# Kernel optimization log

Hardware: AMD Instinct MI355X
Metric: run time of the kernel (lower is better)

The kernel has to match this reference:

```python
import jax, jax.numpy as jnp
import numpy as np

B, R, N, D_IN, D_OUT = 8, 8, 1024, 256, 256


def setup_inputs() -> dict:
    key = jax.random.key(0)
    k1, k2, k3, k4 = jax.random.split(key, 4)
    x = jax.random.normal(k1, (B, N, D_IN), dtype=jnp.float32)
    adj_stack = jax.random.uniform(k2, (B, R, N, N), dtype=jnp.float32)
    # per-relation Linear params, stacked: W[r] maps D_IN -> D_OUT
    bound = 1.0 / np.sqrt(D_IN)
    W = jax.random.uniform(k3, (R, D_IN, D_OUT), minval=-bound, maxval=bound, dtype=jnp.float32)
    b = jax.random.uniform(k4, (R, D_OUT), minval=-bound, maxval=bound, dtype=jnp.float32)
    return {"x": x, "adj_stack": adj_stack, "W": W, "b": b}


def reference(x, adj_stack, W, b):
    # support[b,r,n,e] = x[b,n,:] @ W[r] + b[r]
    support = jnp.einsum('bnd,rde->brne', x, W) + b[None, :, None, :]
    # out[b,m,e] = sum_r adj[b,r,m,:] @ support[b,r,:,e]
    out = jnp.einsum('brmn,brne->bme', adj_stack, support)
    return jax.nn.relu(out)
```

## Files before the change

kernel.cpp:

```cpp
#include <hip/hip_runtime.h>
#include <hip/hip_bf16.h>


#define Bb 8
#define Rr 8
#define Nn 1024
#define Dd 256

typedef __attribute__((ext_vector_type(8))) short short8;
typedef __attribute__((ext_vector_type(4))) short short4v;
typedef __attribute__((ext_vector_type(4))) float f32x4;

__device__ __forceinline__ short f2bf(float f) {
    unsigned u = __builtin_bit_cast(unsigned, f);
    u += 0x7fffu + ((u >> 16) & 1u);
    return (short)(u >> 16);
}

__global__ void prep_w_kernel(const float* __restrict__ W, short* __restrict__ Wt) {
    __shared__ short T[64][72];
    const int tid = threadIdx.x;
    const int et = blockIdx.x, dt = blockIdx.y, r = blockIdx.z;
    const float* Wr = W + ((size_t)r * Dd + dt * 64) * Dd + et * 64;
    #pragma unroll
    for (int i = 0; i < 4; ++i) {
        int idx = tid + i * 256;
        int d_l = idx >> 4;
        int e4  = (idx & 15) * 4;
        f32x4 v = *(const f32x4*)(Wr + d_l * Dd + e4);
        T[e4 + 0][d_l] = f2bf(v[0]);
        T[e4 + 1][d_l] = f2bf(v[1]);
        T[e4 + 2][d_l] = f2bf(v[2]);
        T[e4 + 3][d_l] = f2bf(v[3]);
    }
    __syncthreads();
    short* o = Wt + ((size_t)r * Dd + et * 64) * Dd + dt * 64;
    #pragma unroll
    for (int i = 0; i < 2; ++i) {
        int idx = tid + i * 256;
        int e_l = idx >> 3;
        int d8  = (idx & 7) * 8;
        *(short8*)(o + e_l * Dd + d8) = *(const short8*)&T[e_l][d8];
    }
}

__global__ __launch_bounds__(256) void support_kernel(
        const float* __restrict__ x, const short* __restrict__ Wt,
        const float* __restrict__ bias, short* __restrict__ sup) {
    __shared__ short As[128][40];
    __shared__ short Bs[128][40];

    const int tid = threadIdx.x;
    const int e_t = blockIdx.x, n_t = blockIdx.y, br = blockIdx.z;
    const int b = br >> 3, r = br & 7;
    const int wave = tid >> 6, lane = tid & 63;
    const int quad = lane >> 4, l16 = lane & 15;
    const int we = wave & 1, wn = wave >> 1;

    const short* wp = Wt + ((size_t)r * Dd + e_t * 128) * Dd;
    const float* xb = x + ((size_t)b * Nn + n_t * 128) * Dd;

    short8 aw[2];
    f32x4 xv[4];
    auto load = [&](int d0) {
        #pragma unroll
        for (int i = 0; i < 2; ++i) {
            int idx = tid + i * 256;
            aw[i] = *(const short8*)(wp + (idx >> 2) * Dd + d0 + (idx & 3) * 8);
        }
        #pragma unroll
        for (int i = 0; i < 4; ++i) {
            int idx = tid + i * 256;
            xv[i] = *(const f32x4*)(xb + (idx >> 3) * Dd + d0 + (idx & 7) * 4);
        }
    };

    f32x4 acc[4][4] = {};
    load(0);
    for (int it = 0; it < 8; ++it) {
        #pragma unroll
        for (int i = 0; i < 2; ++i) {
            int idx = tid + i * 256;
            *(short8*)&As[idx >> 2][(idx & 3) * 8] = aw[i];
        }
        #pragma unroll
        for (int i = 0; i < 4; ++i) {
            int idx = tid + i * 256;
            short4v s;
            s[0] = f2bf(xv[i][0]); s[1] = f2bf(xv[i][1]);
            s[2] = f2bf(xv[i][2]); s[3] = f2bf(xv[i][3]);
            *(short4v*)&Bs[idx >> 3][(idx & 7) * 4] = s;
        }
        if (it < 7) load((it + 1) * 32);
        __syncthreads();
        short8 a[4], bfr[4];
        #pragma unroll
        for (int i = 0; i < 4; ++i)
            a[i] = *(const short8*)&As[we * 64 + i * 16 + l16][quad * 8];
        #pragma unroll
        for (int j = 0; j < 4; ++j)
            bfr[j] = *(const short8*)&Bs[wn * 64 + j * 16 + l16][quad * 8];
        #pragma unroll
        for (int i = 0; i < 4; ++i)
            #pragma unroll
            for (int j = 0; j < 4; ++j)
                acc[i][j] = __builtin_amdgcn_mfma_f32_16x16x32_bf16(a[i], bfr[j], acc[i][j], 0, 0, 0);
        __syncthreads();
    }

    #pragma unroll
    for (int i = 0; i < 4; ++i)
        #pragma unroll
        for (int reg = 0; reg < 4; ++reg) {
            int e = e_t * 128 + we * 64 + i * 16 + quad * 4 + reg;
            float bv = bias[r * Dd + e];
            #pragma unroll
            for (int j = 0; j < 4; ++j) {
                int n = n_t * 128 + wn * 64 + j * 16 + l16;
                sup[(((b * Rr + r) * Dd + e) << 10) + n] = f2bf(acc[i][j][reg] + bv);
            }
        }
}

__global__ __launch_bounds__(256) void gcn_gemm_kernel(
        const float* __restrict__ adj, const short* __restrict__ sup,
        float* __restrict__ out) {
    __shared__ short Aa[128][40];
    __shared__ short Bs[128][40];

    const int tid = threadIdx.x;
    const int e2  = blockIdx.x & 1;
    const int r   = blockIdx.x >> 1;
    const int m_t = blockIdx.y, b = blockIdx.z;
    const int wave = tid >> 6, lane = tid & 63;
    const int quad = lane >> 4, l16 = lane & 15;
    const int wm = wave >> 1, we = wave & 1;

    const float* ap = adj + ((size_t)((b * Rr + r) * Nn + m_t * 128)) * Nn;
    const short* bp = sup + (((size_t)((b * Rr + r) * Dd + e2 * 128)) << 10);

    f32x4 av[4];
    short8 bv[2];
    auto load = [&](int n0) {
        #pragma unroll
        for (int i = 0; i < 4; ++i) {
            int idx = tid + i * 256;
            av[i] = *(const f32x4*)(ap + (size_t)(idx >> 3) * Nn + n0 + (idx & 7) * 4);
        }
        #pragma unroll
        for (int i = 0; i < 2; ++i) {
            int idx = tid + i * 256;
            bv[i] = *(const short8*)(bp + ((size_t)(idx >> 2) << 10) + n0 + (idx & 3) * 8);
        }
    };

    f32x4 acc[4][4] = {};
    load(0);
    for (int it = 0; it < 32; ++it) {
        #pragma unroll
        for (int i = 0; i < 4; ++i) {
            int idx = tid + i * 256;
            short4v s;
            s[0] = f2bf(av[i][0]); s[1] = f2bf(av[i][1]);
            s[2] = f2bf(av[i][2]); s[3] = f2bf(av[i][3]);
            *(short4v*)&Aa[idx >> 3][(idx & 7) * 4] = s;
        }
        #pragma unroll
        for (int i = 0; i < 2; ++i) {
            int idx = tid + i * 256;
            *(short8*)&Bs[idx >> 2][(idx & 3) * 8] = bv[i];
        }
        if (it < 31) load((it + 1) * 32);
        __syncthreads();
        short8 a[4], bfr[4];
        #pragma unroll
        for (int i = 0; i < 4; ++i)
            a[i] = *(const short8*)&Aa[wm * 64 + i * 16 + l16][quad * 8];
        #pragma unroll
        for (int j = 0; j < 4; ++j)
            bfr[j] = *(const short8*)&Bs[we * 64 + j * 16 + l16][quad * 8];
        #pragma unroll
        for (int i = 0; i < 4; ++i)
            #pragma unroll
            for (int j = 0; j < 4; ++j)
                acc[i][j] = __builtin_amdgcn_mfma_f32_16x16x32_bf16(a[i], bfr[j], acc[i][j], 0, 0, 0);
        __syncthreads();
    }

    float* ob = out + ((size_t)b * Nn + m_t * 128) * Dd + e2 * 128;
    #pragma unroll
    for (int i = 0; i < 4; ++i)
        #pragma unroll
        for (int reg = 0; reg < 4; ++reg) {
            int m_l = wm * 64 + i * 16 + quad * 4 + reg;
            #pragma unroll
            for (int j = 0; j < 4; ++j) {
                int e_l = we * 64 + j * 16 + l16;
                atomicAdd(ob + (size_t)m_l * Dd + e_l, acc[i][j][reg]);
            }
        }
}

__global__ void relu_kernel(float* __restrict__ out, int n4) {
    int i = blockIdx.x * blockDim.x + threadIdx.x;
    if (i < n4) {
        f32x4* p = (f32x4*)out;
        f32x4 v = p[i];
        v[0] = fmaxf(v[0], 0.f); v[1] = fmaxf(v[1], 0.f);
        v[2] = fmaxf(v[2], 0.f); v[3] = fmaxf(v[3], 0.f);
        p[i] = v;
    }
}

extern "C" void kernel_launch(void* const* d_in, const int* in_sizes, int n_in,
                              void* d_out, int out_size, void* d_ws, size_t ws_size,
                              hipStream_t stream) {
    const float* x    = (const float*)d_in[0];
    const float* adj  = (const float*)d_in[1];
    const float* W    = (const float*)d_in[2];
    const float* bias = (const float*)d_in[3];
    float* out = (float*)d_out;
    short* sup = (short*)d_ws;
    short* Wt  = (short*)d_out;

    prep_w_kernel<<<dim3(4, 4, 8), 256, 0, stream>>>(W, Wt);
    support_kernel<<<dim3(2, 8, 64), 256, 0, stream>>>(x, Wt, bias, sup);
    hipMemsetAsync(d_out, 0, (size_t)out_size * sizeof(float), stream);
    gcn_gemm_kernel<<<dim3(16, 8, 8), 256, 0, stream>>>(adj, sup, out);
    relu_kernel<<<(out_size / 4 + 255) / 256, 256, 0, stream>>>(out, out_size / 4);
}
```

Before: 464.7 us.

## Load MFMA fragments directly from global memory and drop LDS staging

Both GEMM kernels stop staging tiles through shared memory and drop the block barriers. Each wave now loads its A and B fragments from global memory straight into MFMA register layout, converting fp32 to bf16 in registers. Tiles are reshaped so each wave owns a 64-column slice of the output features. In the adjacency GEMM this means all four waves of a block load and convert the same 64x32 adjacency tile, so global/L1 traffic and conversion work are duplicated in exchange for removing LDS writes, LDS reads and barriers.

```diff
diff --git a/kernel.cpp b/kernel.cpp
--- a/kernel.cpp
+++ b/kernel.cpp
@@ -2,13 +2,11 @@
 #include <hip/hip_bf16.h>
 
 
-#define Bb 8
 #define Rr 8
 #define Nn 1024
 #define Dd 256
 
 typedef __attribute__((ext_vector_type(8))) short short8;
-typedef __attribute__((ext_vector_type(4))) short short4v;
 typedef __attribute__((ext_vector_type(4))) float f32x4;
 
 __device__ __forceinline__ short f2bf(float f) {
@@ -38,86 +36,70 @@
     #pragma unroll
     for (int i = 0; i < 2; ++i) {
         int idx = tid + i * 256;
-        int e_l = idx >> 3;
-        int d8  = (idx & 7) * 8;
-        *(short8*)(o + e_l * Dd + d8) = *(const short8*)&T[e_l][d8];
+        *(short8*)(o + (idx >> 3) * Dd + (idx & 7) * 8) = *(const short8*)&T[idx >> 3][(idx & 7) * 8];
     }
 }
 
 __global__ __launch_bounds__(256) void support_kernel(
         const float* __restrict__ x, const short* __restrict__ Wt,
         const float* __restrict__ bias, short* __restrict__ sup) {
-    __shared__ short As[128][40];
-    __shared__ short Bs[128][40];
-
     const int tid = threadIdx.x;
-    const int e_t = blockIdx.x, n_t = blockIdx.y, br = blockIdx.z;
-    const int b = br >> 3, r = br & 7;
     const int wave = tid >> 6, lane = tid & 63;
     const int quad = lane >> 4, l16 = lane & 15;
-    const int we = wave & 1, wn = wave >> 1;
+    const int r = blockIdx.x, n_t = blockIdx.y, b = blockIdx.z;
+    const int e0 = wave * 64, n0 = n_t * 64;
 
-    const short* wp = Wt + ((size_t)r * Dd + e_t * 128) * Dd;
-    const float* xb = x + ((size_t)b * Nn + n_t * 128) * Dd;
+    const short* wp = Wt + (size_t)r * Dd * Dd + (size_t)e0 * Dd;
+    const float* xb = x + ((size_t)b * Nn + n0) * Dd;
 
-    short8 aw[2];
-    f32x4 xv[4];
+    short8 av[4];
+    f32x4 xlo[4], xhi[4];
     auto load = [&](int d0) {
         #pragma unroll
-        for (int i = 0; i < 2; ++i) {
-            int idx = tid + i * 256;
-            aw[i] = *(const short8*)(wp + (idx >> 2) * Dd + d0 + (idx & 3) * 8);
-        }
+        for (int i = 0; i < 4; ++i)
+            av[i] = *(const short8*)(wp + (i * 16 + l16) * Dd + d0 + quad * 8);
         #pragma unroll
-        for (int i = 0; i < 4; ++i) {
-            int idx = tid + i * 256;
-            xv[i] = *(const f32x4*)(xb + (idx >> 3) * Dd + d0 + (idx & 7) * 4);
+        for (int j = 0; j < 4; ++j) {
+            const float* p = xb + (size_t)(j * 16 + l16) * Dd + d0 + quad * 8;
+            xlo[j] = *(const f32x4*)p;
+            xhi[j] = *(const f32x4*)(p + 4);
         }
     };
 
     f32x4 acc[4][4] = {};
     load(0);
     for (int it = 0; it < 8; ++it) {
+        short8 a[4], bfr[4];
         #pragma unroll
-        for (int i = 0; i < 2; ++i) {
-            int idx = tid + i * 256;
-            *(short8*)&As[idx >> 2][(idx & 3) * 8] = aw[i];
-        }
+        for (int i = 0; i < 4; ++i) a[i] = av[i];
         #pragma unroll
-        for (int i = 0; i < 4; ++i) {
-            int idx = tid + i * 256;
-            short4v s;
-            s[0] = f2bf(xv[i][0]); s[1] = f2bf(xv[i][1]);
-            s[2] = f2bf(xv[i][2]); s[3] = f2bf(xv[i][3]);
-            *(short4v*)&Bs[idx >> 3][(idx & 7) * 4] = s;
+        for (int j = 0; j < 4; ++j) {
+            short8 t;
+            t[0] = f2bf(xlo[j][0]); t[1] = f2bf(xlo[j][1]);
+            t[2] = f2bf(xlo[j][2]); t[3] = f2bf(xlo[j][3]);
+            t[4] = f2bf(xhi[j][0]); t[5] = f2bf(xhi[j][1]);
+            t[6] = f2bf(xhi[j][2]); t[7] = f2bf(xhi[j][3]);
+            bfr[j] = t;
         }
         if (it < 7) load((it + 1) * 32);
-        __syncthreads();
-        short8 a[4], bfr[4];
-        #pragma unroll
-        for (int i = 0; i < 4; ++i)
-            a[i] = *(const short8*)&As[we * 64 + i * 16 + l16][quad * 8];
-        #pragma unroll
-        for (int j = 0; j < 4; ++j)
-            bfr[j] = *(const short8*)&Bs[wn * 64 + j * 16 + l16][quad * 8];
         #pragma unroll
         for (int i = 0; i < 4; ++i)
             #pragma unroll
             for (int j = 0; j < 4; ++j)
                 acc[i][j] = __builtin_amdgcn_mfma_f32_16x16x32_bf16(a[i], bfr[j], acc[i][j], 0, 0, 0);
-        __syncthreads();
     }
 
+    short* sb = sup + (((size_t)(b * Rr + r) * Dd) << 10);
     #pragma unroll
     for (int i = 0; i < 4; ++i)
         #pragma unroll
         for (int reg = 0; reg < 4; ++reg) {
-            int e = e_t * 128 + we * 64 + i * 16 + quad * 4 + reg;
+            int e = e0 + i * 16 + quad * 4 + reg;
             float bv = bias[r * Dd + e];
             #pragma unroll
             for (int j = 0; j < 4; ++j) {
-                int n = n_t * 128 + wn * 64 + j * 16 + l16;
-                sup[(((b * Rr + r) * Dd + e) << 10) + n] = f2bf(acc[i][j][reg] + bv);
+                int n = n0 + j * 16 + l16;
+                sb[((size_t)e << 10) + n] = f2bf(acc[i][j][reg] + bv);
             }
         }
 }
@@ -125,79 +107,60 @@
 __global__ __launch_bounds__(256) void gcn_gemm_kernel(
         const float* __restrict__ adj, const short* __restrict__ sup,
         float* __restrict__ out) {
-    __shared__ short Aa[128][40];
-    __shared__ short Bs[128][40];
-
     const int tid = threadIdx.x;
-    const int e2  = blockIdx.x & 1;
-    const int r   = blockIdx.x >> 1;
-    const int m_t = blockIdx.y, b = blockIdx.z;
     const int wave = tid >> 6, lane = tid & 63;
     const int quad = lane >> 4, l16 = lane & 15;
-    const int wm = wave >> 1, we = wave & 1;
+    const int r = blockIdx.x, m_t = blockIdx.y, b = blockIdx.z;
+    const int e0 = wave * 64;
 
-    const float* ap = adj + ((size_t)((b * Rr + r) * Nn + m_t * 128)) * Nn;
-    const short* bp = sup + (((size_t)((b * Rr + r) * Dd + e2 * 128)) << 10);
+    const float* ap = adj + ((size_t)((b * Rr + r) * Nn + m_t * 64)) * Nn;
+    const short* bp = sup + (((size_t)((b * Rr + r) * Dd + e0)) << 10);
 
-    f32x4 av[4];
-    short8 bv[2];
-    auto load = [&](int n0) {
+    f32x4 alo[4], ahi[4];
+    short8 bs[4];
+    auto load = [&](int kk) {
         #pragma unroll
         for (int i = 0; i < 4; ++i) {
-            int idx = tid + i * 256;
-            av[i] = *(const f32x4*)(ap + (size_t)(idx >> 3) * Nn + n0 + (idx & 7) * 4);
+            const float* p = ap + (size_t)(i * 16 + l16) * Nn + kk + quad * 8;
+            alo[i] = *(const f32x4*)p;
+            ahi[i] = *(const f32x4*)(p + 4);
         }
         #pragma unroll
-        for (int i = 0; i < 2; ++i) {
-            int idx = tid + i * 256;
-            bv[i] = *(const short8*)(bp + ((size_t)(idx >> 2) << 10) + n0 + (idx & 3) * 8);
-        }
+        for (int j = 0; j < 4; ++j)
+            bs[j] = *(const short8*)(bp + ((size_t)(j * 16 + l16) << 10) + kk + quad * 8);
     };
 
     f32x4 acc[4][4] = {};
     load(0);
     for (int it = 0; it < 32; ++it) {
+        short8 a[4], bfr[4];
         #pragma unroll
         for (int i = 0; i < 4; ++i) {
-            int idx = tid + i * 256;
-            short4v s;
-            s[0] = f2bf(av[i][0]); s[1] = f2bf(av[i][1]);
-            s[2] = f2bf(av[i][2]); s[3] = f2bf(av[i][3]);
-            *(short4v*)&Aa[idx >> 3][(idx & 7) * 4] = s;
-        }
-        #pragma unroll
-        for (int i = 0; i < 2; ++i) {
-            int idx = tid + i * 256;
-            *(short8*)&Bs[idx >> 2][(idx & 3) * 8] = bv[i];
+            short8 t;
+            t[0] = f2bf(alo[i][0]); t[1] = f2bf(alo[i][1]);
+            t[2] = f2bf(alo[i][2]); t[3] = f2bf(alo[i][3]);
+            t[4] = f2bf(ahi[i][0]); t[5] = f2bf(ahi[i][1]);
+            t[6] = f2bf(ahi[i][2]); t[7] = f2bf(ahi[i][3]);
+            a[i] = t;
+            bfr[i] = bs[i];
         }
         if (it < 31) load((it + 1) * 32);
-        __syncthreads();
-        short8 a[4], bfr[4];
-        #pragma unroll
-        for (int i = 0; i < 4; ++i)
-            a[i] = *(const short8*)&Aa[wm * 64 + i * 16 + l16][quad * 8];
-        #pragma unroll
-        for (int j = 0; j < 4; ++j)
-            bfr[j] = *(const short8*)&Bs[we * 64 + j * 16 + l16][quad * 8];
         #pragma unroll
         for (int i = 0; i < 4; ++i)
             #pragma unroll
             for (int j = 0; j < 4; ++j)
                 acc[i][j] = __builtin_amdgcn_mfma_f32_16x16x32_bf16(a[i], bfr[j], acc[i][j], 0, 0, 0);
-        __syncthreads();
     }
 
-    float* ob = out + ((size_t)b * Nn + m_t * 128) * Dd + e2 * 128;
+    float* ob = out + ((size_t)b * Nn + m_t * 64) * Dd + e0;
     #pragma unroll
     for (int i = 0; i < 4; ++i)
         #pragma unroll
         for (int reg = 0; reg < 4; ++reg) {
-            int m_l = wm * 64 + i * 16 + quad * 4 + reg;
+            int m_l = i * 16 + quad * 4 + reg;
             #pragma unroll
-            for (int j = 0; j < 4; ++j) {
-                int e_l = we * 64 + j * 16 + l16;
-                atomicAdd(ob + (size_t)m_l * Dd + e_l, acc[i][j][reg]);
-            }
+            for (int j = 0; j < 4; ++j)
+                atomicAdd(ob + (size_t)m_l * Dd + j * 16 + l16, acc[i][j][reg]);
         }
 }
 
@@ -224,8 +187,8 @@
     short* Wt  = (short*)d_out;
 
     prep_w_kernel<<<dim3(4, 4, 8), 256, 0, stream>>>(W, Wt);
-    support_kernel<<<dim3(2, 8, 64), 256, 0, stream>>>(x, Wt, bias, sup);
+    support_kernel<<<dim3(8, 16, 8), 256, 0, stream>>>(x, Wt, bias, sup);
     hipMemsetAsync(d_out, 0, (size_t)out_size * sizeof(float), stream);
-    gcn_gemm_kernel<<<dim3(16, 8, 8), 256, 0, stream>>>(adj, sup, out);
+    gcn_gemm_kernel<<<dim3(8, 16, 8), 256, 0, stream>>>(adj, sup, out);
     relu_kernel<<<(out_size / 4 + 255) / 256, 256, 0, stream>>>(out, out_size / 4);
 }
```

Measured after the change: 545.8 us. 17.5% more time.

## Load GEMM tiles directly into LDS via global_load_lds and convert after LDS

Applied to the files above, without the earlier changes.

Both GEMM kernels now fetch A and B tiles with the direct global-to-LDS load builtin instead of staging through registers. The fp32 operand (x or adj) is stored raw in LDS and converted to bf16 when fragments are read. Launch bounds now request 3 blocks per SM. The register-based prefetch and software pipelining are gone. LDS padding is removed, which risks bank conflicts, and the fp32 tile doubles LDS footprint, so loads are no longer overlapped with MFMA across iterations.

```diff
diff --git a/kernel.cpp b/kernel.cpp
--- a/kernel.cpp
+++ b/kernel.cpp
@@ -2,19 +2,23 @@
 #include <hip/hip_bf16.h>
 
 
-#define Bb 8
 #define Rr 8
 #define Nn 1024
 #define Dd 256
 
 typedef __attribute__((ext_vector_type(8))) short short8;
-typedef __attribute__((ext_vector_type(4))) short short4v;
 typedef __attribute__((ext_vector_type(4))) float f32x4;
 
 __device__ __forceinline__ short f2bf(float f) {
     unsigned u = __builtin_bit_cast(unsigned, f);
     u += 0x7fffu + ((u >> 16) & 1u);
     return (short)(u >> 16);
+}
+
+__device__ __forceinline__ void gload_lds16(const void* g, void* l) {
+    __builtin_amdgcn_global_load_lds(
+        (const __attribute__((address_space(1))) unsigned int*)g,
+        (__attribute__((address_space(3))) unsigned int*)l, 16, 0, 0);
 }
 
 __global__ void prep_w_kernel(const float* __restrict__ W, short* __restrict__ Wt) {
@@ -38,68 +42,56 @@
     #pragma unroll
     for (int i = 0; i < 2; ++i) {
         int idx = tid + i * 256;
-        int e_l = idx >> 3;
-        int d8  = (idx & 7) * 8;
-        *(short8*)(o + e_l * Dd + d8) = *(const short8*)&T[e_l][d8];
-    }
-}
-
-__global__ __launch_bounds__(256) void support_kernel(
+        *(short8*)(o + (idx >> 3) * Dd + (idx & 7) * 8) = *(const short8*)&T[idx >> 3][(idx & 7) * 8];
+    }
+}
+
+__global__ __launch_bounds__(256, 3) void support_kernel(
         const float* __restrict__ x, const short* __restrict__ Wt,
         const float* __restrict__ bias, short* __restrict__ sup) {
-    __shared__ short As[128][40];
-    __shared__ short Bs[128][40];
+    __shared__ short As[128 * 32];
+    __shared__ float Bs[128 * 32];
 
     const int tid = threadIdx.x;
+    const int wave = tid >> 6, lane = tid & 63;
+    const int quad = lane >> 4, l16 = lane & 15;
     const int e_t = blockIdx.x, n_t = blockIdx.y, br = blockIdx.z;
     const int b = br >> 3, r = br & 7;
-    const int wave = tid >> 6, lane = tid & 63;
-    const int quad = lane >> 4, l16 = lane & 15;
     const int we = wave & 1, wn = wave >> 1;
 
     const short* wp = Wt + ((size_t)r * Dd + e_t * 128) * Dd;
     const float* xb = x + ((size_t)b * Nn + n_t * 128) * Dd;
 
-    short8 aw[2];
-    f32x4 xv[4];
-    auto load = [&](int d0) {
+    f32x4 acc[4][4] = {};
+
+    for (int it = 0; it < 8; ++it) {
+        const int d0 = it * 32;
         #pragma unroll
         for (int i = 0; i < 2; ++i) {
-            int idx = tid + i * 256;
-            aw[i] = *(const short8*)(wp + (idx >> 2) * Dd + d0 + (idx & 3) * 8);
+            int row = 16 * wave + 64 * i;
+            gload_lds16(wp + (size_t)(row + (lane >> 2)) * Dd + d0 + (lane & 3) * 8,
+                        &As[row * 32]);
         }
         #pragma unroll
         for (int i = 0; i < 4; ++i) {
-            int idx = tid + i * 256;
-            xv[i] = *(const f32x4*)(xb + (idx >> 3) * Dd + d0 + (idx & 7) * 4);
-        }
-    };
-
-    f32x4 acc[4][4] = {};
-    load(0);
-    for (int it = 0; it < 8; ++it) {
-        #pragma unroll
-        for (int i = 0; i < 2; ++i) {
-            int idx = tid + i * 256;
-            *(short8*)&As[idx >> 2][(idx & 3) * 8] = aw[i];
-        }
-        #pragma unroll
-        for (int i = 0; i < 4; ++i) {
-            int idx = tid + i * 256;
-            short4v s;
-            s[0] = f2bf(xv[i][0]); s[1] = f2bf(xv[i][1]);
-            s[2] = f2bf(xv[i][2]); s[3] = f2bf(xv[i][3]);
-            *(short4v*)&Bs[idx >> 3][(idx & 7) * 4] = s;
-        }
-        if (it < 7) load((it + 1) * 32);
+            int row = 8 * wave + 32 * i;
+            gload_lds16(xb + (size_t)(row + (lane >> 3)) * Dd + d0 + (lane & 7) * 4,
+                        &Bs[row * 32]);
+        }
         __syncthreads();
         short8 a[4], bfr[4];
         #pragma unroll
         for (int i = 0; i < 4; ++i)
-            a[i] = *(const short8*)&As[we * 64 + i * 16 + l16][quad * 8];
-        #pragma unroll
-        for (int j = 0; j < 4; ++j)
-            bfr[j] = *(const short8*)&Bs[wn * 64 + j * 16 + l16][quad * 8];
+            a[i] = *(const short8*)&As[(we * 64 + i * 16 + l16) * 32 + quad * 8];
+        #pragma unroll
+        for (int j = 0; j < 4; ++j) {
+            const float* p = &Bs[(wn * 64 + j * 16 + l16) * 32 + quad * 8];
+            f32x4 lo = *(const f32x4*)p, hi = *(const f32x4*)(p + 4);
+            short8 t;
+            t[0] = f2bf(lo[0]); t[1] = f2bf(lo[1]); t[2] = f2bf(lo[2]); t[3] = f2bf(lo[3]);
+            t[4] = f2bf(hi[0]); t[5] = f2bf(hi[1]); t[6] = f2bf(hi[2]); t[7] = f2bf(hi[3]);
+            bfr[j] = t;
+        }
         #pragma unroll
         for (int i = 0; i < 4; ++i)
             #pragma unroll
@@ -122,63 +114,52 @@
         }
 }
 
-__global__ __launch_bounds__(256) void gcn_gemm_kernel(
+__global__ __launch_bounds__(256, 3) void gcn_gemm_kernel(
         const float* __restrict__ adj, const short* __restrict__ sup,
         float* __restrict__ out) {
-    __shared__ short Aa[128][40];
-    __shared__ short Bs[128][40];
+    __shared__ float Aa[128 * 32];
+    __shared__ short Bs[128 * 32];
 
     const int tid = threadIdx.x;
-    const int e2  = blockIdx.x & 1;
-    const int r   = blockIdx.x >> 1;
-    const int m_t = blockIdx.y, b = blockIdx.z;
     const int wave = tid >> 6, lane = tid & 63;
     const int quad = lane >> 4, l16 = lane & 15;
+    const int e2 = blockIdx.x & 1, r = blockIdx.x >> 1;
+    const int m_t = blockIdx.y, b = blockIdx.z;
     const int wm = wave >> 1, we = wave & 1;
 
     const float* ap = adj + ((size_t)((b * Rr + r) * Nn + m_t * 128)) * Nn;
     const short* bp = sup + (((size_t)((b * Rr + r) * Dd + e2 * 128)) << 10);
 
-    f32x4 av[4];
-    short8 bv[2];
-    auto load = [&](int n0) {
+    f32x4 acc[4][4] = {};
+
+    for (int it = 0; it < 32; ++it) {
+        const int kk = it * 32;
         #pragma unroll
         for (int i = 0; i < 4; ++i) {
-            int idx = tid + i * 256;
-            av[i] = *(const f32x4*)(ap + (size_t)(idx >> 3) * Nn + n0 + (idx & 7) * 4);
+            int row = 8 * wave + 32 * i;
+            gload_lds16(ap + (size_t)(row + (lane >> 3)) * Nn + kk + (lane & 7) * 4,
+                        &Aa[row * 32]);
         }
         #pragma unroll
         for (int i = 0; i < 2; ++i) {
-            int idx = tid + i * 256;
-            bv[i] = *(const short8*)(bp + ((size_t)(idx >> 2) << 10) + n0 + (idx & 3) * 8);
-        }
-    };
-
-    f32x4 acc[4][4] = {};
-    load(0);
-    for (int it = 0; it < 32; ++it) {
+            int row = 16 * wave + 64 * i;
+            gload_lds16(bp + (((size_t)(row + (lane >> 2))) << 10) + kk + (lane & 3) * 8,
+                        &Bs[row * 32]);
+        }
+        __syncthreads();
+        short8 a[4], bfr[4];
         #pragma unroll
         for (int i = 0; i < 4; ++i) {
-            int idx = tid + i * 256;
-            short4v s;
-            s[0] = f2bf(av[i][0]); s[1] = f2bf(av[i][1]);
-            s[2] = f2bf(av[i][2]); s[3] = f2bf(av[i][3]);
-            *(short4v*)&Aa[idx >> 3][(idx & 7) * 4] = s;
-        }
-        #pragma unroll
-        for (int i = 0; i < 2; ++i) {
-            int idx = tid + i * 256;
-            *(short8*)&Bs[idx >> 2][(idx & 3) * 8] = bv[i];
-        }
-        if (it < 31) load((it + 1) * 32);
-        __syncthreads();
-        short8 a[4], bfr[4];
-        #pragma unroll
-        for (int i = 0; i < 4; ++i)
-            a[i] = *(const short8*)&Aa[wm * 64 + i * 16 + l16][quad * 8];
+            const float* p = &Aa[(wm * 64 + i * 16 + l16) * 32 + quad * 8];
+            f32x4 lo = *(const f32x4*)p, hi = *(const f32x4*)(p + 4);
+            short8 t;
+            t[0] = f2bf(lo[0]); t[1] = f2bf(lo[1]); t[2] = f2bf(lo[2]); t[3] = f2bf(lo[3]);
+            t[4] = f2bf(hi[0]); t[5] = f2bf(hi[1]); t[6] = f2bf(hi[2]); t[7] = f2bf(hi[3]);
+            a[i] = t;
+        }
         #pragma unroll
         for (int j = 0; j < 4; ++j)
-            bfr[j] = *(const short8*)&Bs[we * 64 + j * 16 + l16][quad * 8];
+            bfr[j] = *(const short8*)&Bs[(we * 64 + j * 16 + l16) * 32 + quad * 8];
         #pragma unroll
         for (int i = 0; i < 4; ++i)
             #pragma unroll
@@ -194,10 +175,8 @@
         for (int reg = 0; reg < 4; ++reg) {
             int m_l = wm * 64 + i * 16 + quad * 4 + reg;
             #pragma unroll
-            for (int j = 0; j < 4; ++j) {
-                int e_l = we * 64 + j * 16 + l16;
-                atomicAdd(ob + (size_t)m_l * Dd + e_l, acc[i][j][reg]);
-            }
+            for (int j = 0; j < 4; ++j)
+                atomicAdd(ob + (size_t)m_l * Dd + we * 64 + j * 16 + l16, acc[i][j][reg]);
         }
 }
 
```

New measurement: 458.9 us. No clear change (-1.2%).
